# Kernel tuning notes

Measured on AMD Instinct MI355X. Metric: run time of the kernel, lower is better.

## Reference

```python
import jax, jax.numpy as jnp
import numpy as np

N = 100000
E = 1600000
IN_C, HID_C, OUT_C = 128, 128, 64


def setup_inputs() -> dict:
    key = jax.random.key(0)
    k_x, k_e, k1, k2 = jax.random.split(key, 4)
    x = jax.random.normal(k_x, (N, IN_C), dtype=jnp.float32)
    edge_index = jax.random.randint(k_e, (2, E), 0, N, dtype=jnp.int32)
    # Glorot-style init for GCN weights, zero bias (PyG default)
    W1 = jax.random.normal(k1, (IN_C, HID_C), dtype=jnp.float32) * (1.0 / np.sqrt(IN_C))
    b1 = jnp.zeros((HID_C,), dtype=jnp.float32)
    W2 = jax.random.normal(k2, (HID_C, OUT_C), dtype=jnp.float32) * (1.0 / np.sqrt(HID_C))
    b2 = jnp.zeros((OUT_C,), dtype=jnp.float32)
    return {"x": x, "edge_index": edge_index, "W1": W1, "b1": b1, "W2": W2, "b2": b2}


def _gcn_norm(edge_index, n):
    # PyG gcn_norm: add self-loops, symmetric normalization D^-1/2 A D^-1/2
    loops = jnp.arange(n, dtype=edge_index.dtype)
    row = jnp.concatenate([edge_index[0], loops])  # source nodes
    col = jnp.concatenate([edge_index[1], loops])  # target nodes
    deg = jax.ops.segment_sum(jnp.ones_like(col, dtype=jnp.float32), col, num_segments=n)
    dinv = jnp.where(deg > 0, jax.lax.rsqrt(deg), 0.0)
    norm = dinv[row] * dinv[col]  # [E + N]
    return row, col, norm


def _gcn_conv(h, W, b, row, col, norm, n):
    h = h @ W                              # dense transform first (out_c <= in_c)
    msg = h[row] * norm[:, None]           # gather + scale per edge
    agg = jax.ops.segment_sum(msg, col, num_segments=n)  # scatter-add at targets
    return agg + b


def reference(x, edge_index, W1, b1, W2, b2):
    n = x.shape[0]
    row, col, norm = _gcn_norm(edge_index, n)
    h = jax.nn.relu(_gcn_conv(x, W1, b1, row, col, norm, n))
    mu = _gcn_conv(h, W2, b2, row, col, norm, n)
    return mu
```

## Files before the change

### kernel.cpp

```cpp
#include <hip/hip_runtime.h>
#include <hip/hip_bf16.h>


static inline int cdiv(int a, int b) { return (a + b - 1) / b; }

__device__ inline unsigned short f2bf(float f) {
    __hip_bfloat16 b = __float2bfloat16(f);
    return *(unsigned short*)&b;
}
__device__ inline float2 bf2_to_f2(unsigned int u) {
    return make_float2(__uint_as_float(u << 16),
                       __uint_as_float(u & 0xffff0000u));
}
__device__ inline float bf_to_f(unsigned short u) {
    return __uint_as_float(((unsigned int)u) << 16);
}


__global__ void k_init(int* __restrict__ cnt, int* __restrict__ cursor, int n) {
    int i = blockIdx.x * blockDim.x + threadIdx.x;
    if (i < n) { cnt[i] = 0; cursor[i] = 0; }
}

__global__ void k_deg(const int* __restrict__ col, int* __restrict__ cnt, int e) {
    int i = blockIdx.x * blockDim.x + threadIdx.x;
    if (i < e) atomicAdd(&cnt[col[i]], 1);
}

__global__ void k_dinv(const int* __restrict__ cnt, float* __restrict__ dinv, int n) {
    int i = blockIdx.x * blockDim.x + threadIdx.x;
    if (i < n) dinv[i] = rsqrtf((float)(cnt[i] + 1));
}

__global__ void k_scan1(const int* __restrict__ cnt, int* __restrict__ pref,
                        int* __restrict__ bsum, int n) {
    __shared__ int s[256];
    int t = threadIdx.x;
    int i = blockIdx.x * 256 + t;
    int v = (i < n) ? cnt[i] : 0;
    s[t] = v;
    __syncthreads();
    for (int off = 1; off < 256; off <<= 1) {
        int x = (t >= off) ? s[t - off] : 0;
        __syncthreads();
        s[t] += x;
        __syncthreads();
    }
    if (i < n) pref[i] = s[t] - v;
    if (t == 255) bsum[blockIdx.x] = s[255];
}

__global__ void k_scan2(const int* __restrict__ bsum, int* __restrict__ boff, int nb) {
    __shared__ int s[512];
    int t = threadIdx.x;
    int v = (t < nb) ? bsum[t] : 0;
    s[t] = v;
    __syncthreads();
    for (int off = 1; off < 512; off <<= 1) {
        int x = (t >= off) ? s[t - off] : 0;
        __syncthreads();
        s[t] += x;
        __syncthreads();
    }
    if (t < nb) boff[t] = s[t] - v;
}

__global__ void k_scan3(int* __restrict__ pref, const int* __restrict__ boff,
                        int n, int e_total) {
    int i = blockIdx.x * blockDim.x + threadIdx.x;
    if (i < n) pref[i] += boff[i >> 8];
    if (i == n) pref[n] = e_total;
}

__global__ void k_fill(const int* __restrict__ row, const int* __restrict__ col,
                       const int* __restrict__ indptr, int* __restrict__ cursor,
                       const float* __restrict__ dinv,
                       int2* __restrict__ csr, int e) {
    int i = blockIdx.x * blockDim.x + threadIdx.x;
    if (i >= e) return;
    int c = col[i], r = row[i];
    int pos = indptr[c] + atomicAdd(&cursor[c], 1);
    csr[pos] = make_int2(r, __float_as_int(dinv[r] * dinv[c]));
}


template <int COUT>
__global__ __launch_bounds__(256) void gemm_k(const float* __restrict__ X,
                                              const float* __restrict__ W,
                                              __hip_bfloat16* __restrict__ H, int n) {
    constexpr int KT = 64;
    constexpr int CG = COUT / 4;
    constexpr int MG = 256 / CG;
    constexpr int TILE_M = MG * 4;
    __shared__ float xs[TILE_M][KT];
    __shared__ float ws[KT][COUT];
    const int t = threadIdx.x;
    const int m_base = blockIdx.x * TILE_M;
    const int tx = t % CG, ty = t / CG;
    const int c0 = tx * 4, m0 = ty * 4;
    float acc[4][4] = {};
    for (int kt = 0; kt < 128; kt += KT) {
        {
            const float4* src = (const float4*)(W + (size_t)kt * COUT);
            float4* dst = (float4*)&ws[0][0];
            constexpr int NW = KT * COUT / 4 / 256;
#pragma unroll
            for (int i = 0; i < NW; i++) dst[t + i * 256] = src[t + i * 256];
        }
        {
            float4* dst = (float4*)&xs[0][0];
            constexpr int NX = TILE_M * KT / 4 / 256;
#pragma unroll
            for (int i = 0; i < NX; i++) {
                int idx = t + i * 256;
                int m = idx >> 4, q = idx & 15;
                int gm = m_base + m;
                float4 v = make_float4(0.f, 0.f, 0.f, 0.f);
                if (gm < n) v = ((const float4*)X)[(size_t)gm * 32 + (kt >> 2) + q];
                dst[idx] = v;
            }
        }
        __syncthreads();
#pragma unroll
        for (int k = 0; k < KT; k += 4) {
            float xr[4][4], wr[4][4];
#pragma unroll
            for (int mm = 0; mm < 4; mm++) {
                float4 v = *(const float4*)&xs[m0 + mm][k];
                xr[mm][0] = v.x; xr[mm][1] = v.y; xr[mm][2] = v.z; xr[mm][3] = v.w;
            }
#pragma unroll
            for (int kk = 0; kk < 4; kk++) {
                float4 v = *(const float4*)&ws[k + kk][c0];
                wr[kk][0] = v.x; wr[kk][1] = v.y; wr[kk][2] = v.z; wr[kk][3] = v.w;
            }
#pragma unroll
            for (int kk = 0; kk < 4; kk++)
#pragma unroll
                for (int mm = 0; mm < 4; mm++)
#pragma unroll
                    for (int cc = 0; cc < 4; cc++)
                        acc[mm][cc] = fmaf(xr[mm][kk], wr[kk][cc], acc[mm][cc]);
        }
        __syncthreads();
    }
#pragma unroll
    for (int mm = 0; mm < 4; mm++) {
        int gm = m_base + m0 + mm;
        if (gm < n) {
            ushort4 o;
            o.x = f2bf(acc[mm][0]); o.y = f2bf(acc[mm][1]);
            o.z = f2bf(acc[mm][2]); o.w = f2bf(acc[mm][3]);
            *(ushort4*)&H[(size_t)gm * COUT + c0] = o;
        }
    }
}


__global__ __launch_bounds__(256) void k_agg128(const __hip_bfloat16* __restrict__ h,
                                                const int* __restrict__ indptr,
                                                const int2* __restrict__ csr,
                                                const float* __restrict__ dinv,
                                                const float* __restrict__ bias,
                                                float* __restrict__ out, int n) {
    int wid = (blockIdx.x * blockDim.x + threadIdx.x) >> 6;
    int lane = threadIdx.x & 63;
    if (wid >= n) return;
    const unsigned int* hp = (const unsigned int*)h;
    float di = dinv[wid];
    float wself = di * di;
    float2 hv = bf2_to_f2(hp[(size_t)wid * 64 + lane]);
    float2 a[8];
#pragma unroll
    for (int k = 0; k < 8; k++) a[k] = make_float2(0.f, 0.f);
    a[0].x = wself * hv.x;
    a[0].y = wself * hv.y;
    int e = indptr[wid], e1 = indptr[wid + 1];
    for (; e + 8 <= e1; e += 8) {
        int2 c[8];
#pragma unroll
        for (int k = 0; k < 8; k++) c[k] = csr[e + k];
#pragma unroll
        for (int k = 0; k < 8; k++) {
            float nr = __int_as_float(c[k].y);
            float2 v = bf2_to_f2(hp[(size_t)c[k].x * 64 + lane]);
            a[k].x = fmaf(nr, v.x, a[k].x);
            a[k].y = fmaf(nr, v.y, a[k].y);
        }
    }
    for (; e < e1; e++) {
        int2 ck = csr[e];
        float nr = __int_as_float(ck.y);
        float2 v = bf2_to_f2(hp[(size_t)ck.x * 64 + lane]);
        a[0].x = fmaf(nr, v.x, a[0].x);
        a[0].y = fmaf(nr, v.y, a[0].y);
    }
    float sx = ((a[0].x + a[1].x) + (a[2].x + a[3].x)) +
               ((a[4].x + a[5].x) + (a[6].x + a[7].x));
    float sy = ((a[0].y + a[1].y) + (a[2].y + a[3].y)) +
               ((a[4].y + a[5].y) + (a[6].y + a[7].y));
    float2 b = ((const float2*)bias)[lane];
    ((float2*)(out + (size_t)wid * 128))[lane] =
        make_float2(fmaxf(sx + b.x, 0.f), fmaxf(sy + b.y, 0.f));
}

__global__ __launch_bounds__(256) void k_agg64(const __hip_bfloat16* __restrict__ h,
                                               const int* __restrict__ indptr,
                                               const int2* __restrict__ csr,
                                               const float* __restrict__ dinv,
                                               const float* __restrict__ bias,
                                               float* __restrict__ out, int n) {
    int wid = (blockIdx.x * blockDim.x + threadIdx.x) >> 6;
    int lane = threadIdx.x & 63;
    if (wid >= n) return;
    const unsigned short* hp = (const unsigned short*)h;
    float di = dinv[wid];
    float a[8];
#pragma unroll
    for (int k = 0; k < 8; k++) a[k] = 0.f;
    a[0] = di * di * bf_to_f(hp[(size_t)wid * 64 + lane]);
    int e = indptr[wid], e1 = indptr[wid + 1];
    for (; e + 8 <= e1; e += 8) {
        int2 c[8];
#pragma unroll
        for (int k = 0; k < 8; k++) c[k] = csr[e + k];
#pragma unroll
        for (int k = 0; k < 8; k++) {
            float nr = __int_as_float(c[k].y);
            a[k] = fmaf(nr, bf_to_f(hp[(size_t)c[k].x * 64 + lane]), a[k]);
        }
    }
    for (; e < e1; e++) {
        int2 ck = csr[e];
        float nr = __int_as_float(ck.y);
        a[0] = fmaf(nr, bf_to_f(hp[(size_t)ck.x * 64 + lane]), a[0]);
    }
    float s = ((a[0] + a[1]) + (a[2] + a[3])) + ((a[4] + a[5]) + (a[6] + a[7]));
    out[(size_t)wid * 64 + lane] = s + bias[lane];
}


extern "C" void kernel_launch(void* const* d_in, const int* in_sizes, int n_in,
                              void* d_out, int out_size, void* d_ws, size_t ws_size,
                              hipStream_t stream) {
    const float* x  = (const float*)d_in[0];
    const int* ei   = (const int*)d_in[1];
    const float* W1 = (const float*)d_in[2];
    const float* b1 = (const float*)d_in[3];
    const float* W2 = (const float*)d_in[4];
    const float* b2 = (const float*)d_in[5];
    float* out = (float*)d_out;

    const int N = in_sizes[0] / 128;
    const int E = in_sizes[1] / 2;
    const int* row = ei;
    const int* col = ei + E;

    char* p = (char*)d_ws;
    auto carve = [&](size_t bytes) -> void* {
        void* r = (void*)p;
        p += (bytes + 255) & ~(size_t)255;
        return r;
    };
    int*   cnt      = (int*)carve((size_t)N * 4);
    float* dinv     = (float*)carve((size_t)N * 4);
    int*   indptr   = (int*)carve((size_t)(N + 1) * 4);
    int*   bsum     = (int*)carve(512 * 4);
    int*   boff     = (int*)carve(512 * 4);
    int*   cursor   = (int*)carve((size_t)N * 4);
    int2*  csr      = (int2*)carve((size_t)E * 8);
    __hip_bfloat16* h  = (__hip_bfloat16*)carve((size_t)N * 128 * 2);
    float* h1          = (float*)carve((size_t)N * 128 * 4);
    __hip_bfloat16* h2 = (__hip_bfloat16*)carve((size_t)N * 64 * 2);

    const int NB = cdiv(N, 256);

    k_init<<<cdiv(N, 256), 256, 0, stream>>>(cnt, cursor, N);
    k_deg<<<cdiv(E, 256), 256, 0, stream>>>(col, cnt, E);
    k_dinv<<<cdiv(N, 256), 256, 0, stream>>>(cnt, dinv, N);
    k_scan1<<<NB, 256, 0, stream>>>(cnt, indptr, bsum, N);
    k_scan2<<<1, 512, 0, stream>>>(bsum, boff, NB);
    k_scan3<<<cdiv(N + 1, 256), 256, 0, stream>>>(indptr, boff, N, E);
    k_fill<<<cdiv(E, 256), 256, 0, stream>>>(row, col, indptr, cursor, dinv,
                                             csr, E);

    gemm_k<128><<<cdiv(N, 32), 256, 0, stream>>>(x, W1, h, N);
    k_agg128<<<cdiv(N, 4), 256, 0, stream>>>(h, indptr, csr, dinv, b1, h1, N);
    gemm_k<64><<<cdiv(N, 64), 256, 0, stream>>>(h1, W2, h2, N);
    k_agg64<<<cdiv(N, 4), 256, 0, stream>>>(h2, indptr, csr, dinv, b2, out, N);
}
```

Measured before the change: 470.1 us.

## Factor symmetric normalization into GEMM epilogue and aggregation output, drop per-edge weights

Instead of storing a per-edge normalization weight in the CSR, the source-side dinv scale is applied in the GEMM epilogue and the target-side dinv is applied once per node after aggregation. The CSR shrinks from int2 to a single int row index, which halves index traffic in the fill and in both aggregations and removes the dinv gathers from k_fill. The aggregation loops are unrolled to 16 edges with 4 partial accumulators. The pre-scaled features are rounded to bf16 after scaling, which changes rounding slightly.

```diff
diff --git a/kernel.cpp b/kernel.cpp
--- a/kernel.cpp
+++ b/kernel.cpp
@@ -74,20 +74,20 @@
 
 __global__ void k_fill(const int* __restrict__ row, const int* __restrict__ col,
                        const int* __restrict__ indptr, int* __restrict__ cursor,
-                       const float* __restrict__ dinv,
-                       int2* __restrict__ csr, int e) {
+                       int* __restrict__ csr_row, int e) {
     int i = blockIdx.x * blockDim.x + threadIdx.x;
     if (i >= e) return;
-    int c = col[i], r = row[i];
+    int c = col[i];
     int pos = indptr[c] + atomicAdd(&cursor[c], 1);
-    csr[pos] = make_int2(r, __float_as_int(dinv[r] * dinv[c]));
+    csr_row[pos] = row[i];
 }
 
 
 template <int COUT>
 __global__ __launch_bounds__(256) void gemm_k(const float* __restrict__ X,
                                               const float* __restrict__ W,
-                                              __hip_bfloat16* __restrict__ H, int n) {
+                                              const float* __restrict__ dinv,
+                                              __hip_bfloat16* __restrict__ G, int n) {
     constexpr int KT = 64;
     constexpr int CG = COUT / 4;
     constexpr int MG = 256 / CG;
@@ -148,95 +148,86 @@
     for (int mm = 0; mm < 4; mm++) {
         int gm = m_base + m0 + mm;
         if (gm < n) {
+            float dv = dinv[gm];
             ushort4 o;
-            o.x = f2bf(acc[mm][0]); o.y = f2bf(acc[mm][1]);
-            o.z = f2bf(acc[mm][2]); o.w = f2bf(acc[mm][3]);
-            *(ushort4*)&H[(size_t)gm * COUT + c0] = o;
-        }
-    }
-}
-
-
-__global__ __launch_bounds__(256) void k_agg128(const __hip_bfloat16* __restrict__ h,
+            o.x = f2bf(dv * acc[mm][0]); o.y = f2bf(dv * acc[mm][1]);
+            o.z = f2bf(dv * acc[mm][2]); o.w = f2bf(dv * acc[mm][3]);
+            *(ushort4*)&G[(size_t)gm * COUT + c0] = o;
+        }
+    }
+}
+
+
+__global__ __launch_bounds__(256) void k_agg128(const __hip_bfloat16* __restrict__ g,
                                                 const int* __restrict__ indptr,
-                                                const int2* __restrict__ csr,
+                                                const int* __restrict__ csr_row,
                                                 const float* __restrict__ dinv,
                                                 const float* __restrict__ bias,
                                                 float* __restrict__ out, int n) {
     int wid = (blockIdx.x * blockDim.x + threadIdx.x) >> 6;
     int lane = threadIdx.x & 63;
     if (wid >= n) return;
-    const unsigned int* hp = (const unsigned int*)h;
-    float di = dinv[wid];
-    float wself = di * di;
-    float2 hv = bf2_to_f2(hp[(size_t)wid * 64 + lane]);
-    float2 a[8];
-#pragma unroll
-    for (int k = 0; k < 8; k++) a[k] = make_float2(0.f, 0.f);
-    a[0].x = wself * hv.x;
-    a[0].y = wself * hv.y;
+    const unsigned int* gp = (const unsigned int*)g;
+    float2 a[4];
+#pragma unroll
+    for (int k = 0; k < 4; k++) a[k] = make_float2(0.f, 0.f);
+    {
+        float2 v = bf2_to_f2(gp[(size_t)wid * 64 + lane]);
+        a[0].x = v.x; a[0].y = v.y;
+    }
     int e = indptr[wid], e1 = indptr[wid + 1];
-    for (; e + 8 <= e1; e += 8) {
-        int2 c[8];
-#pragma unroll
-        for (int k = 0; k < 8; k++) c[k] = csr[e + k];
-#pragma unroll
-        for (int k = 0; k < 8; k++) {
-            float nr = __int_as_float(c[k].y);
-            float2 v = bf2_to_f2(hp[(size_t)c[k].x * 64 + lane]);
-            a[k].x = fmaf(nr, v.x, a[k].x);
-            a[k].y = fmaf(nr, v.y, a[k].y);
+    for (; e + 16 <= e1; e += 16) {
+        int r[16];
+#pragma unroll
+        for (int k = 0; k < 16; k++) r[k] = csr_row[e + k];
+#pragma unroll
+        for (int k = 0; k < 16; k++) {
+            float2 v = bf2_to_f2(gp[(size_t)r[k] * 64 + lane]);
+            a[k & 3].x += v.x;
+            a[k & 3].y += v.y;
         }
     }
     for (; e < e1; e++) {
-        int2 ck = csr[e];
-        float nr = __int_as_float(ck.y);
-        float2 v = bf2_to_f2(hp[(size_t)ck.x * 64 + lane]);
-        a[0].x = fmaf(nr, v.x, a[0].x);
-        a[0].y = fmaf(nr, v.y, a[0].y);
-    }
-    float sx = ((a[0].x + a[1].x) + (a[2].x + a[3].x)) +
-               ((a[4].x + a[5].x) + (a[6].x + a[7].x));
-    float sy = ((a[0].y + a[1].y) + (a[2].y + a[3].y)) +
-               ((a[4].y + a[5].y) + (a[6].y + a[7].y));
+        int r = csr_row[e];
+        float2 v = bf2_to_f2(gp[(size_t)r * 64 + lane]);
+        a[0].x += v.x;
+        a[0].y += v.y;
+    }
+    float dv = dinv[wid];
+    float sx = (a[0].x + a[1].x) + (a[2].x + a[3].x);
+    float sy = (a[0].y + a[1].y) + (a[2].y + a[3].y);
     float2 b = ((const float2*)bias)[lane];
     ((float2*)(out + (size_t)wid * 128))[lane] =
-        make_float2(fmaxf(sx + b.x, 0.f), fmaxf(sy + b.y, 0.f));
-}
-
-__global__ __launch_bounds__(256) void k_agg64(const __hip_bfloat16* __restrict__ h,
+        make_float2(fmaxf(fmaf(dv, sx, b.x), 0.f), fmaxf(fmaf(dv, sy, b.y), 0.f));
+}
+
+__global__ __launch_bounds__(256) void k_agg64(const __hip_bfloat16* __restrict__ g,
                                                const int* __restrict__ indptr,
-                                               const int2* __restrict__ csr,
+                                               const int* __restrict__ csr_row,
                                                const float* __restrict__ dinv,
                                                const float* __restrict__ bias,
                                                float* __restrict__ out, int n) {
     int wid = (blockIdx.x * blockDim.x + threadIdx.x) >> 6;
     int lane = threadIdx.x & 63;
     if (wid >= n) return;
-    const unsigned short* hp = (const unsigned short*)h;
-    float di = dinv[wid];
-    float a[8];
-#pragma unroll
-    for (int k = 0; k < 8; k++) a[k] = 0.f;
-    a[0] = di * di * bf_to_f(hp[(size_t)wid * 64 + lane]);
+    const unsigned short* gp = (const unsigned short*)g;
+    float a[4];
+#pragma unroll
+    for (int k = 0; k < 4; k++) a[k] = 0.f;
+    a[0] = bf_to_f(gp[(size_t)wid * 64 + lane]);
     int e = indptr[wid], e1 = indptr[wid + 1];
-    for (; e + 8 <= e1; e += 8) {
-        int2 c[8];
-#pragma unroll
-        for (int k = 0; k < 8; k++) c[k] = csr[e + k];
-#pragma unroll
-        for (int k = 0; k < 8; k++) {
-            float nr = __int_as_float(c[k].y);
-            a[k] = fmaf(nr, bf_to_f(hp[(size_t)c[k].x * 64 + lane]), a[k]);
-        }
-    }
-    for (; e < e1; e++) {
-        int2 ck = csr[e];
-        float nr = __int_as_float(ck.y);
-        a[0] = fmaf(nr, bf_to_f(hp[(size_t)ck.x * 64 + lane]), a[0]);
-    }
-    float s = ((a[0] + a[1]) + (a[2] + a[3])) + ((a[4] + a[5]) + (a[6] + a[7]));
-    out[(size_t)wid * 64 + lane] = s + bias[lane];
+    for (; e + 16 <= e1; e += 16) {
+        int r[16];
+#pragma unroll
+        for (int k = 0; k < 16; k++) r[k] = csr_row[e + k];
+#pragma unroll
+        for (int k = 0; k < 16; k++)
+            a[k & 3] += bf_to_f(gp[(size_t)r[k] * 64 + lane]);
+    }
+    for (; e < e1; e++)
+        a[0] += bf_to_f(gp[(size_t)csr_row[e] * 64 + lane]);
+    float s = (a[0] + a[1]) + (a[2] + a[3]);
+    out[(size_t)wid * 64 + lane] = fmaf(dinv[wid], s, bias[lane]);
 }
 
 
@@ -268,10 +259,10 @@
     int*   bsum     = (int*)carve(512 * 4);
     int*   boff     = (int*)carve(512 * 4);
     int*   cursor   = (int*)carve((size_t)N * 4);
-    int2*  csr      = (int2*)carve((size_t)E * 8);
-    __hip_bfloat16* h  = (__hip_bfloat16*)carve((size_t)N * 128 * 2);
+    int*   csr_row  = (int*)carve((size_t)E * 4);
+    __hip_bfloat16* g1 = (__hip_bfloat16*)carve((size_t)N * 128 * 2);
     float* h1          = (float*)carve((size_t)N * 128 * 4);
-    __hip_bfloat16* h2 = (__hip_bfloat16*)carve((size_t)N * 64 * 2);
+    __hip_bfloat16* g2 = (__hip_bfloat16*)carve((size_t)N * 64 * 2);
 
     const int NB = cdiv(N, 256);
 
@@ -281,11 +272,10 @@
     k_scan1<<<NB, 256, 0, stream>>>(cnt, indptr, bsum, N);
     k_scan2<<<1, 512, 0, stream>>>(bsum, boff, NB);
     k_scan3<<<cdiv(N + 1, 256), 256, 0, stream>>>(indptr, boff, N, E);
-    k_fill<<<cdiv(E, 256), 256, 0, stream>>>(row, col, indptr, cursor, dinv,
-                                             csr, E);
-
-    gemm_k<128><<<cdiv(N, 32), 256, 0, stream>>>(x, W1, h, N);
-    k_agg128<<<cdiv(N, 4), 256, 0, stream>>>(h, indptr, csr, dinv, b1, h1, N);
-    gemm_k<64><<<cdiv(N, 64), 256, 0, stream>>>(h1, W2, h2, N);
-    k_agg64<<<cdiv(N, 4), 256, 0, stream>>>(h2, indptr, csr, dinv, b2, out, N);
-}
+    k_fill<<<cdiv(E, 256), 256, 0, stream>>>(row, col, indptr, cursor, csr_row, E);
+
+    gemm_k<128><<<cdiv(N, 32), 256, 0, stream>>>(x, W1, dinv, g1, N);
+    k_agg128<<<cdiv(N, 4), 256, 0, stream>>>(g1, indptr, csr_row, dinv, b1, h1, N);
+    gemm_k<64><<<cdiv(N, 64), 256, 0, stream>>>(h1, W2, dinv, g2, N);
+    k_agg64<<<cdiv(N, 4), 256, 0, stream>>>(g2, indptr, csr_row, dinv, b2, out, N);
+}
```

After: 529.3 us. +12.6%, slower.
